# Kernel optimization log

Hardware: AMD Instinct MI355X
Metric: run time of the kernel (lower is better)

The kernel has to match this reference:

```python
import jax, jax.numpy as jnp
import numpy as np

B, T, D, H = 2, 2048, 2048, 16
HD = D // H
EPS = 1e-8
NEG = -1e9


def setup_inputs() -> dict:
    key = jax.random.key(0)
    ks = jax.random.split(key, 6)
    x = jax.random.normal(ks[0], (B, T, D), dtype=jnp.float32)
    # additive causal mask, broadcast over [B, H, T, T]
    causal = jnp.tril(jnp.ones((T, T), dtype=bool))
    attn_mask = jnp.where(causal, 0.0, NEG).astype(jnp.float32)[None, None]
    s = 1.0 / np.sqrt(D)
    w_norm = jnp.ones((D,), dtype=jnp.float32)
    wq = jax.random.normal(ks[1], (D, D), dtype=jnp.float32) * s
    wk = jax.random.normal(ks[2], (D, D), dtype=jnp.float32) * s
    wv = jax.random.normal(ks[3], (D, D), dtype=jnp.float32) * s
    wo = jax.random.normal(ks[4], (D, D), dtype=jnp.float32) * s
    return {"x": x, "attn_mask": attn_mask, "w_norm": w_norm,
            "wq": wq, "wk": wk, "wv": wv, "wo": wo}


def _rmsnorm(x, w):
    # norm = ||x||_2 * D^-0.5 ; out = w * x / (norm + eps)  (eps outside, as in source)
    norm = jnp.sqrt(jnp.sum(x * x, axis=-1, keepdims=True)) * (x.shape[-1] ** -0.5)
    return w * x / (norm + EPS)


def reference(x, attn_mask, w_norm, wq, wk, wv, wo):
    b, t, d = x.shape
    xn = _rmsnorm(x, w_norm)
    # Linear (no bias): y = x @ W^T ; split into heads -> [B, H, T, HD]
    def proj(w):
        return jnp.einsum('btd,ed->bte', xn, w).reshape(b, t, H, HD).transpose(0, 2, 1, 3)
    q, k, v = proj(wq), proj(wk), proj(wv)
    scale = HD ** -0.5
    w_scores = jnp.einsum('bhqd,bhkd->bhqk', q, k) * scale + attn_mask
    p = jax.nn.softmax(w_scores, axis=-1)
    out = jnp.einsum('bhqk,bhkd->bhqd', p, v)
    out = out.transpose(0, 2, 1, 3).reshape(b, t, d)
    return jnp.einsum('btd,ed->bte', out, wo)
```

## Files before the change

kernel.cpp:

```cpp
#include <hip/hip_runtime.h>
#include <stdint.h>

#define TT 2048
#define DD 2048
#define NHH 16
#define HDD 128
#define BTT 4096

typedef __attribute__((ext_vector_type(8))) short bf16x8;
typedef __attribute__((ext_vector_type(4))) float f32x4;

__device__ __forceinline__ unsigned short f2bf(float f) {
    union { float f; uint32_t u; } v; v.f = f;
    uint32_t u = v.u;
    u += 0x7fffu + ((u >> 16) & 1u);
    return (unsigned short)(u >> 16);
}

__device__ __forceinline__ void gld16(const unsigned short* g, unsigned short* l) {
    __builtin_amdgcn_global_load_lds(
        (const __attribute__((address_space(1))) unsigned int*)g,
        (__attribute__((address_space(3))) unsigned int*)l, 16, 0, 0);
}

__global__ __launch_bounds__(256) void convert_w(const float* __restrict__ wq,
                                                 const float* __restrict__ wk,
                                                 const float* __restrict__ wv,
                                                 const float* __restrict__ wo,
                                                 unsigned short* __restrict__ out) {
    size_t gid = (size_t)blockIdx.x * 256 + threadIdx.x;
    size_t base = gid * 8;
    int which = (int)(base >> 22);
    const float* src = which == 0 ? wq : which == 1 ? wk : which == 2 ? wv : wo;
    size_t off = base & 4194303u;
    float4 a = ((const float4*)(src + off))[0];
    float4 b = ((const float4*)(src + off))[1];
    union { unsigned short us[8]; uint4 v; } pk;
    pk.us[0] = f2bf(a.x); pk.us[1] = f2bf(a.y); pk.us[2] = f2bf(a.z); pk.us[3] = f2bf(a.w);
    pk.us[4] = f2bf(b.x); pk.us[5] = f2bf(b.y); pk.us[6] = f2bf(b.z); pk.us[7] = f2bf(b.w);
    *(uint4*)(out + base) = pk.v;
}

__global__ __launch_bounds__(256) void rmsnorm_k(const float* __restrict__ x,
                                                 const float* __restrict__ w,
                                                 unsigned short* __restrict__ xn) {
    const int row = blockIdx.x;
    const int tid = threadIdx.x;
    const float* xr = x + (size_t)row * DD;
    float4 a = ((const float4*)xr)[tid * 2];
    float4 b = ((const float4*)xr)[tid * 2 + 1];
    float ss = a.x*a.x + a.y*a.y + a.z*a.z + a.w*a.w
             + b.x*b.x + b.y*b.y + b.z*b.z + b.w*b.w;
    #pragma unroll
    for (int m = 1; m < 64; m <<= 1) ss += __shfl_xor(ss, m, 64);
    __shared__ float wss[4];
    if ((tid & 63) == 0) wss[tid >> 6] = ss;
    __syncthreads();
    float total = wss[0] + wss[1] + wss[2] + wss[3];
    float norm = sqrtf(total) * 0.022097086912079612f;
    float inv = 1.0f / (norm + 1e-8f);
    float4 wa = ((const float4*)w)[tid * 2];
    float4 wb = ((const float4*)w)[tid * 2 + 1];
    union { unsigned short us[8]; uint4 v; } pk;
    pk.us[0] = f2bf(wa.x * a.x * inv); pk.us[1] = f2bf(wa.y * a.y * inv);
    pk.us[2] = f2bf(wa.z * a.z * inv); pk.us[3] = f2bf(wa.w * a.w * inv);
    pk.us[4] = f2bf(wb.x * b.x * inv); pk.us[5] = f2bf(wb.y * b.y * inv);
    pk.us[6] = f2bf(wb.z * b.z * inv); pk.us[7] = f2bf(wb.w * b.w * inv);
    ((uint4*)(xn + (size_t)row * DD))[tid] = pk.v;
}

__device__ __forceinline__ void gemm_core(const unsigned short* __restrict__ Ag0,
                                          const unsigned short* __restrict__ Bg0,
                                          unsigned short* As, unsigned short* Bs,
                                          int tid, f32x4 acc[4][4]) {
    const int w = tid >> 6, lane = tid & 63;
    const int l15 = lane & 15, lq = lane >> 4;
    const int wr = (w >> 1) * 64, wc = (w & 1) * 64;
    const unsigned short* ag = Ag0 + (size_t)(w * 16 + (lane >> 2)) * DD + (lane & 3) * 8;
    const unsigned short* bg = Bg0 + (size_t)(w * 16 + (lane >> 2)) * DD + (lane & 3) * 8;
    unsigned short* al = As + w * 512;
    unsigned short* bl = Bs + w * 512;
    for (int k0 = 0; k0 < DD; k0 += 32) {
        __syncthreads();
        gld16(ag + k0, al);
        gld16(ag + k0 + (size_t)64 * DD, al + 64 * 32);
        gld16(bg + k0, bl);
        gld16(bg + k0 + (size_t)64 * DD, bl + 64 * 32);
        __syncthreads();
        bf16x8 af[4], bfr[4];
        #pragma unroll
        for (int i = 0; i < 4; i++)
            af[i] = *(const bf16x8*)(As + (wr + i * 16 + l15) * 32 + lq * 8);
        #pragma unroll
        for (int j = 0; j < 4; j++)
            bfr[j] = *(const bf16x8*)(Bs + (wc + j * 16 + l15) * 32 + lq * 8);
        #pragma unroll
        for (int i = 0; i < 4; i++)
            #pragma unroll
            for (int j = 0; j < 4; j++)
                acc[i][j] = __builtin_amdgcn_mfma_f32_16x16x32_bf16(af[i], bfr[j], acc[i][j], 0, 0, 0);
    }
}

__global__ __launch_bounds__(256) void gemm_qkv(const unsigned short* __restrict__ A,
                                                const unsigned short* __restrict__ W3,
                                                unsigned short* __restrict__ O3) {
    __shared__ __align__(16) unsigned short As[128 * 32];
    __shared__ __align__(16) unsigned short Bs[128 * 32];
    const int tid = threadIdx.x;
    const int wave = tid >> 6, lane = tid & 63;
    const int l15 = lane & 15, lq = lane >> 4;
    const int by = blockIdx.y;
    const int which = by >> 4;
    const unsigned short* Bw = W3 + (size_t)which * DD * DD;
    unsigned short* C = O3 + (size_t)which * BTT * DD;
    const int m0 = blockIdx.x * 128, n0 = (by & 15) * 128;
    const int wr = (wave >> 1) * 64, wc = (wave & 1) * 64;
    const f32x4 zf = {0.f, 0.f, 0.f, 0.f};
    f32x4 acc[4][4];
    #pragma unroll
    for (int i = 0; i < 4; i++)
        #pragma unroll
        for (int j = 0; j < 4; j++) acc[i][j] = zf;
    gemm_core(A + (size_t)m0 * DD, Bw + (size_t)n0 * DD, As, Bs, tid, acc);
    #pragma unroll
    for (int i = 0; i < 4; i++) {
        const int row = m0 + wr + i * 16 + lq * 4;
        #pragma unroll
        for (int j = 0; j < 4; j++) {
            const int col = n0 + wc + j * 16 + l15;
            #pragma unroll
            for (int r = 0; r < 4; r++)
                C[(size_t)(row + r) * DD + col] = f2bf(acc[i][j][r]);
        }
    }
}

__global__ __launch_bounds__(256) void gemm_out(const unsigned short* __restrict__ A,
                                                const unsigned short* __restrict__ Bw,
                                                float* __restrict__ C) {
    __shared__ __align__(16) unsigned short As[128 * 32];
    __shared__ __align__(16) unsigned short Bs[128 * 32];
    const int tid = threadIdx.x;
    const int wave = tid >> 6, lane = tid & 63;
    const int l15 = lane & 15, lq = lane >> 4;
    const int m0 = blockIdx.x * 128, n0 = blockIdx.y * 128;
    const int wr = (wave >> 1) * 64, wc = (wave & 1) * 64;
    const f32x4 zf = {0.f, 0.f, 0.f, 0.f};
    f32x4 acc[4][4];
    #pragma unroll
    for (int i = 0; i < 4; i++)
        #pragma unroll
        for (int j = 0; j < 4; j++) acc[i][j] = zf;
    gemm_core(A + (size_t)m0 * DD, Bw + (size_t)n0 * DD, As, Bs, tid, acc);
    #pragma unroll
    for (int i = 0; i < 4; i++) {
        const int row = m0 + wr + i * 16 + lq * 4;
        #pragma unroll
        for (int j = 0; j < 4; j++) {
            const int col = n0 + wc + j * 16 + l15;
            #pragma unroll
            for (int r = 0; r < 4; r++)
                C[(size_t)(row + r) * DD + col] = acc[i][j][r];
        }
    }
}

__global__ __launch_bounds__(256) void attn_fused(const unsigned short* __restrict__ q,
                                                  const unsigned short* __restrict__ k,
                                                  const unsigned short* __restrict__ v,
                                                  unsigned short* __restrict__ o) {
    constexpr int LKK = 136;
    constexpr int LPP = 72;
    __shared__ __align__(16) unsigned short Ks[2][64 * LKK];
    __shared__ __align__(16) unsigned short Vts[128 * 64];
    __shared__ __align__(16) unsigned short Ps[4 * 16 * LPP];
    const int h = blockIdx.y, b = blockIdx.z;
    const int tid = threadIdx.x, wave = tid >> 6, lane = tid & 63;
    const int l15 = lane & 15, lq = lane >> 4;
    const size_t rowbase = (size_t)b * TT;
    const int hcol = h * HDD;
    const float scale = 0.08838834764831845f;
    unsigned short* Pw = Ps + wave * 16 * LPP;
    const f32x4 zf = {0.f, 0.f, 0.f, 0.f};

    uint4 kr0, kr1, kr2, kr3, vr0, vr1, vr2, vr3;
    const int sidx = tid * 8;
    const int srr = sidx >> 7;
    const int sc  = sidx & 127;
    const int swz = ((sc >> 3) & 7) << 3;
    const int srs0 = (srr +  0) ^ swz;
    const int srs1 = (srr + 16) ^ swz;
    const int srs2 = (srr + 32) ^ swz;
    const int srs3 = (srr + 48) ^ swz;

    for (int half = 0; half < 2; half++) {
        const int qj = (half == 0) ? blockIdx.x : 31 - blockIdx.x;
        const int qt0 = qj * 64;
        bf16x8 aq[4];
        {
            const unsigned short* qrp = q + (rowbase + qt0 + wave * 16 + l15) * DD + hcol;
            #pragma unroll
            for (int kk = 0; kk < 4; kk++)
                aq[kk] = *(const bf16x8*)(qrp + kk * 32 + lq * 8);
        }
        f32x4 acc_o[8];
        #pragma unroll
        for (int jh = 0; jh < 8; jh++) acc_o[jh] = zf;
        float m_i[4], l_i[4];
        #pragma unroll
        for (int r = 0; r < 4; r++) { m_i[r] = -1e30f; l_i[r] = 0.f; }
        const int qp0 = qt0 + wave * 16 + lq * 4;
        const int nkt = qj + 1;

        __syncthreads();
        {
            const unsigned short* kg = k + rowbase * DD + hcol;
            const unsigned short* vg = v + rowbase * DD + hcol;
            kr0 = *(const uint4*)(kg + (size_t)(srr +  0) * DD + sc);
            kr1 = *(const uint4*)(kg + (size_t)(srr + 16) * DD + sc);
            kr2 = *(const uint4*)(kg + (size_t)(srr + 32) * DD + sc);
            kr3 = *(const uint4*)(kg + (size_t)(srr + 48) * DD + sc);
            vr0 = *(const uint4*)(vg + (size_t)(srr +  0) * DD + sc);
            vr1 = *(const uint4*)(vg + (size_t)(srr + 16) * DD + sc);
            vr2 = *(const uint4*)(vg + (size_t)(srr + 32) * DD + sc);
            vr3 = *(const uint4*)(vg + (size_t)(srr + 48) * DD + sc);
            unsigned short* ksb = &Ks[0][0];
            *(uint4*)(ksb + (srr +  0) * LKK + sc) = kr0;
            *(uint4*)(ksb + (srr + 16) * LKK + sc) = kr1;
            *(uint4*)(ksb + (srr + 32) * LKK + sc) = kr2;
            *(uint4*)(ksb + (srr + 48) * LKK + sc) = kr3;
            if (nkt > 1) {
                const unsigned short* kg1 = k + (rowbase + 64) * DD + hcol;
                kr0 = *(const uint4*)(kg1 + (size_t)(srr +  0) * DD + sc);
                kr1 = *(const uint4*)(kg1 + (size_t)(srr + 16) * DD + sc);
                kr2 = *(const uint4*)(kg1 + (size_t)(srr + 32) * DD + sc);
                kr3 = *(const uint4*)(kg1 + (size_t)(srr + 48) * DD + sc);
            }
        }

        for (int kt = 0; kt < nkt; kt++) {
            const int cur = kt & 1;
            __syncthreads();
            {
                const unsigned short* d0 = (const unsigned short*)&vr0;
                const unsigned short* d1 = (const unsigned short*)&vr1;
                const unsigned short* d2 = (const unsigned short*)&vr2;
                const unsigned short* d3 = (const unsigned short*)&vr3;
                #pragma unroll
                for (int jj = 0; jj < 8; jj++) {
                    Vts[(sc + jj) * 64 + srs0] = d0[jj];
                    Vts[(sc + jj) * 64 + srs1] = d1[jj];
                    Vts[(sc + jj) * 64 + srs2] = d2[jj];
                    Vts[(sc + jj) * 64 + srs3] = d3[jj];
                }
            }
            if (kt + 1 < nkt) {
                unsigned short* ksb = &Ks[cur ^ 1][0];
                *(uint4*)(ksb + (srr +  0) * LKK + sc) = kr0;
                *(uint4*)(ksb + (srr + 16) * LKK + sc) = kr1;
                *(uint4*)(ksb + (srr + 32) * LKK + sc) = kr2;
                *(uint4*)(ksb + (srr + 48) * LKK + sc) = kr3;
            }
            if (kt + 2 < nkt) {
                const unsigned short* kg = k + (rowbase + (kt + 2) * 64) * DD + hcol;
                kr0 = *(const uint4*)(kg + (size_t)(srr +  0) * DD + sc);
                kr1 = *(const uint4*)(kg + (size_t)(srr + 16) * DD + sc);
                kr2 = *(const uint4*)(kg + (size_t)(srr + 32) * DD + sc);
                kr3 = *(const uint4*)(kg + (size_t)(srr + 48) * DD + sc);
            }
            if (kt + 1 < nkt) {
                const unsigned short* vg = v + (rowbase + (kt + 1) * 64) * DD + hcol;
                vr0 = *(const uint4*)(vg + (size_t)(srr +  0) * DD + sc);
                vr1 = *(const uint4*)(vg + (size_t)(srr + 16) * DD + sc);
                vr2 = *(const uint4*)(vg + (size_t)(srr + 32) * DD + sc);
                vr3 = *(const uint4*)(vg + (size_t)(srr + 48) * DD + sc);
            }
            const unsigned short* ksc = &Ks[cur][0];
            f32x4 accs[4];
            #pragma unroll
            for (int j = 0; j < 4; j++) accs[j] = zf;
            __builtin_amdgcn_s_setprio(1);
            #pragma unroll
            for (int j = 0; j < 4; j++)
                #pragma unroll
                for (int kk = 0; kk < 4; kk++) {
                    bf16x8 bk = *(const bf16x8*)(&ksc[(j * 16 + l15) * LKK + kk * 32 + lq * 8]);
                    accs[j] = __builtin_amdgcn_mfma_f32_16x16x32_bf16(aq[kk], bk, accs[j], 0, 0, 0);
                }
            __builtin_amdgcn_s_setprio(0);
            const int kbase = kt * 64;
            float rowmax[4] = {-1e30f, -1e30f, -1e30f, -1e30f};
            #pragma unroll
            for (int j = 0; j < 4; j++) {
                const int kp = kbase + j * 16 + l15;
                #pragma unroll
                for (int r = 0; r < 4; r++) {
                    float s = accs[j][r] * scale;
                    s = (kp > qp0 + r) ? -1e30f : s;
                    accs[j][r] = s;
                    rowmax[r] = fmaxf(rowmax[r], s);
                }
            }
            #pragma unroll
            for (int r = 0; r < 4; r++) {
                float mx = rowmax[r];
                mx = fmaxf(mx, __shfl_xor(mx, 1, 64));
                mx = fmaxf(mx, __shfl_xor(mx, 2, 64));
                mx = fmaxf(mx, __shfl_xor(mx, 4, 64));
                mx = fmaxf(mx, __shfl_xor(mx, 8, 64));
                float m_new = fmaxf(m_i[r], mx);
                float al = __expf(m_i[r] - m_new);
                m_i[r] = m_new;
                l_i[r] *= al;
                #pragma unroll
                for (int jh = 0; jh < 8; jh++) acc_o[jh][r] *= al;
            }
            float rowsum[4] = {0.f, 0.f, 0.f, 0.f};
            #pragma unroll
            for (int j = 0; j < 4; j++)
                #pragma unroll
                for (int r = 0; r < 4; r++) {
                    float p = __expf(accs[j][r] - m_i[r]);
                    rowsum[r] += p;
                    Pw[(lq * 4 + r) * LPP + j * 16 + l15] = f2bf(p);
                }
            #pragma unroll
            for (int r = 0; r < 4; r++) {
                float s = rowsum[r];
                s += __shfl_xor(s, 1, 64);
                s += __shfl_xor(s, 2, 64);
                s += __shfl_xor(s, 4, 64);
                s += __shfl_xor(s, 8, 64);
                l_i[r] += s;
            }
            __syncthreads();
            bf16x8 ap[2];
            #pragma unroll
            for (int kk = 0; kk < 2; kk++)
                ap[kk] = *(const bf16x8*)(&Pw[l15 * LPP + kk * 32 + lq * 8]);
            __builtin_amdgcn_s_setprio(1);
            #pragma unroll
            for (int jh = 0; jh < 8; jh++) {
                const int hd = jh * 16 + l15;
                const int vswz = ((hd >> 3) & 7) << 3;
                #pragma unroll
                for (int kk = 0; kk < 2; kk++) {
                    bf16x8 bv = *(const bf16x8*)(&Vts[hd * 64 + ((kk * 32 + lq * 8) ^ vswz)]);
                    acc_o[jh] = __builtin_amdgcn_mfma_f32_16x16x32_bf16(ap[kk], bv, acc_o[jh], 0, 0, 0);
                }
            }
            __builtin_amdgcn_s_setprio(0);
        }
        #pragma unroll
        for (int jh = 0; jh < 8; jh++) {
            const int col = hcol + jh * 16 + l15;
            #pragma unroll
            for (int r = 0; r < 4; r++)
                o[(rowbase + qp0 + r) * DD + col] = f2bf(acc_o[jh][r] * (1.0f / l_i[r]));
        }
    }
}

extern "C" void kernel_launch(void* const* d_in, const int* in_sizes, int n_in,
                              void* d_out, int out_size, void* d_ws, size_t ws_size,
                              hipStream_t stream) {
    const float* x      = (const float*)d_in[0];
    const float* w_norm = (const float*)d_in[2];
    const float* wq     = (const float*)d_in[3];
    const float* wk     = (const float*)d_in[4];
    const float* wv     = (const float*)d_in[5];
    const float* wo     = (const float*)d_in[6];

    unsigned short* wbf = (unsigned short*)d_ws;
    unsigned short* xn  = wbf + (size_t)4 * DD * DD;
    unsigned short* qb  = xn + (size_t)BTT * DD;
    unsigned short* kb  = qb + (size_t)BTT * DD;
    unsigned short* vb  = kb + (size_t)BTT * DD;
    unsigned short* ab  = vb + (size_t)BTT * DD;

    convert_w<<<8192, 256, 0, stream>>>(wq, wk, wv, wo, wbf);
    rmsnorm_k<<<BTT, 256, 0, stream>>>(x, w_norm, xn);
    dim3 gqkv(32, 48);
    gemm_qkv<<<gqkv, 256, 0, stream>>>(xn, wbf, qb);
    dim3 gattn(16, NHH, 2);
    attn_fused<<<gattn, 256, 0, stream>>>(qb, kb, vb, ab);
    dim3 gout(32, 16);
    gemm_out<<<gout, 256, 0, stream>>>(ab, wbf + (size_t)3 * DD * DD, (float*)d_out);
}
```

Baseline: 423.8 us.

## Rewrite projection GEMMs with 256x256 tiles, double-buffered swizzled LDS and grid remap

Replaces the 128x128, 4-wave GEMM core with a 256x256, 8-wave core. It uses BK=64, double-buffered 128KB LDS with XOR-swizzled layout, and interleaves global_load_lds prefetch of the next K tile with MFMA quadrants. It also remaps workgroup IDs for L2 locality. The aim is more reuse per loaded byte, less LDS bank conflicts, and overlap of memory with compute in the QKV and output projections. The cost is higher register and LDS pressure and fewer workgroups (384 and 128), which may underfill the 256 CUs for the output GEMM.

Result: slower. 445.8 us (+5.2%).

```diff
diff --git a/kernel.cpp b/kernel.cpp
--- a/kernel.cpp
+++ b/kernel.cpp
@@ -9,6 +9,8 @@
 
 typedef __attribute__((ext_vector_type(8))) short bf16x8;
 typedef __attribute__((ext_vector_type(4))) float f32x4;
+
+#define MF(a, b, c) __builtin_amdgcn_mfma_f32_16x16x32_bf16(a, b, c, 0, 0, 0)
 
 __device__ __forceinline__ unsigned short f2bf(float f) {
     union { float f; uint32_t u; } v; v.f = f;
@@ -69,99 +71,198 @@
     ((uint4*)(xn + (size_t)row * DD))[tid] = pk.v;
 }
 
-__device__ __forceinline__ void gemm_core(const unsigned short* __restrict__ Ag0,
-                                          const unsigned short* __restrict__ Bg0,
-                                          unsigned short* As, unsigned short* Bs,
-                                          int tid, f32x4 acc[4][4]) {
-    const int w = tid >> 6, lane = tid & 63;
-    const int l15 = lane & 15, lq = lane >> 4;
-    const int wr = (w >> 1) * 64, wc = (w & 1) * 64;
-    const unsigned short* ag = Ag0 + (size_t)(w * 16 + (lane >> 2)) * DD + (lane & 3) * 8;
-    const unsigned short* bg = Bg0 + (size_t)(w * 16 + (lane >> 2)) * DD + (lane & 3) * 8;
-    unsigned short* al = As + w * 512;
-    unsigned short* bl = Bs + w * 512;
-    for (int k0 = 0; k0 < DD; k0 += 32) {
-        __syncthreads();
-        gld16(ag + k0, al);
-        gld16(ag + k0 + (size_t)64 * DD, al + 64 * 32);
-        gld16(bg + k0, bl);
-        gld16(bg + k0 + (size_t)64 * DD, bl + 64 * 32);
-        __syncthreads();
-        bf16x8 af[4], bfr[4];
-        #pragma unroll
-        for (int i = 0; i < 4; i++)
-            af[i] = *(const bf16x8*)(As + (wr + i * 16 + l15) * 32 + lq * 8);
-        #pragma unroll
-        for (int j = 0; j < 4; j++)
-            bfr[j] = *(const bf16x8*)(Bs + (wc + j * 16 + l15) * 32 + lq * 8);
-        #pragma unroll
-        for (int i = 0; i < 4; i++)
-            #pragma unroll
-            for (int j = 0; j < 4; j++)
-                acc[i][j] = __builtin_amdgcn_mfma_f32_16x16x32_bf16(af[i], bfr[j], acc[i][j], 0, 0, 0);
-    }
-}
-
-__global__ __launch_bounds__(256) void gemm_qkv(const unsigned short* __restrict__ A,
-                                                const unsigned short* __restrict__ W3,
-                                                unsigned short* __restrict__ O3) {
-    __shared__ __align__(16) unsigned short As[128 * 32];
-    __shared__ __align__(16) unsigned short Bs[128 * 32];
+__device__ __forceinline__ void gemm256_core(const unsigned short* __restrict__ Ag,
+                                             const unsigned short* __restrict__ Bg,
+                                             unsigned short* lds, f32x4 acc[8][4]) {
     const int tid = threadIdx.x;
     const int wave = tid >> 6, lane = tid & 63;
-    const int l15 = lane & 15, lq = lane >> 4;
-    const int by = blockIdx.y;
-    const int which = by >> 4;
+    const int wm = wave >> 2, wn = wave & 3;
+    const int l15 = lane & 15, lq = lane >> 4, r7 = l15 & 7;
+    const int gr = lane >> 3;
+    const size_t goff = (size_t)gr * DD + (size_t)((((lane & 7) ^ gr)) * 8);
+    const int xk0 = (lq ^ r7) * 8;
+    const int xk1 = ((4 + lq) ^ r7) * 8;
+    const int aro = (wm * 128 + l15) * 64;
+    const int bro = 16384 + (wn * 64 + l15) * 64;
+    const int sw16 = wave * 16;
+
+    #pragma unroll
+    for (int c = 0; c < 2; c++) {
+        gld16(Ag + (size_t)(sw16 + c * 8) * DD + goff,       lds + (sw16 + c * 8) * 64);
+        gld16(Ag + (size_t)(128 + sw16 + c * 8) * DD + goff, lds + (128 + sw16 + c * 8) * 64);
+        gld16(Bg + (size_t)(sw16 + c * 8) * DD + goff,       lds + 16384 + (sw16 + c * 8) * 64);
+        gld16(Bg + (size_t)(128 + sw16 + c * 8) * DD + goff, lds + 16384 + (128 + sw16 + c * 8) * 64);
+    }
+    asm volatile("s_waitcnt vmcnt(0)" ::: "memory");
+    __builtin_amdgcn_sched_barrier(0);
+    __builtin_amdgcn_s_barrier();
+
+    for (int kt = 0; kt < DD / 64; kt++) {
+        const int cur = (kt & 1) << 15;
+        const int nxt = cur ^ 32768;
+        const bool hn = (kt + 1 < DD / 64);
+        const int kn = (kt + 1) * 64;
+        const unsigned short* ac = lds + cur + aro;
+        const unsigned short* bc = lds + cur + bro;
+        bf16x8 af[4][2], bA[2][2], bB[2][2];
+
+        #pragma unroll
+        for (int m = 0; m < 4; m++) {
+            af[m][0] = *(const bf16x8*)(ac + m * 1024 + xk0);
+            af[m][1] = *(const bf16x8*)(ac + m * 1024 + xk1);
+        }
+        #pragma unroll
+        for (int n = 0; n < 2; n++) {
+            bA[n][0] = *(const bf16x8*)(bc + n * 1024 + xk0);
+            bA[n][1] = *(const bf16x8*)(bc + n * 1024 + xk1);
+        }
+        if (hn) {
+            gld16(Ag + (size_t)(sw16 + 0) * DD + kn + goff, lds + nxt + (sw16 + 0) * 64);
+            gld16(Ag + (size_t)(sw16 + 8) * DD + kn + goff, lds + nxt + (sw16 + 8) * 64);
+        }
+        __builtin_amdgcn_s_barrier();
+        asm volatile("s_waitcnt lgkmcnt(0)" ::: "memory");
+        __builtin_amdgcn_sched_barrier(0);
+        __builtin_amdgcn_s_setprio(1);
+        #pragma unroll
+        for (int m = 0; m < 4; m++)
+            #pragma unroll
+            for (int n = 0; n < 2; n++) {
+                acc[m][n] = MF(af[m][0], bA[n][0], acc[m][n]);
+                acc[m][n] = MF(af[m][1], bA[n][1], acc[m][n]);
+            }
+        __builtin_amdgcn_s_setprio(0);
+        __builtin_amdgcn_s_barrier();
+
+        #pragma unroll
+        for (int n = 0; n < 2; n++) {
+            bB[n][0] = *(const bf16x8*)(bc + (2 + n) * 1024 + xk0);
+            bB[n][1] = *(const bf16x8*)(bc + (2 + n) * 1024 + xk1);
+        }
+        if (hn) {
+            gld16(Ag + (size_t)(128 + sw16 + 0) * DD + kn + goff, lds + nxt + (128 + sw16 + 0) * 64);
+            gld16(Ag + (size_t)(128 + sw16 + 8) * DD + kn + goff, lds + nxt + (128 + sw16 + 8) * 64);
+        }
+        __builtin_amdgcn_s_barrier();
+        asm volatile("s_waitcnt lgkmcnt(0)" ::: "memory");
+        __builtin_amdgcn_sched_barrier(0);
+        __builtin_amdgcn_s_setprio(1);
+        #pragma unroll
+        for (int m = 0; m < 4; m++)
+            #pragma unroll
+            for (int n = 0; n < 2; n++) {
+                acc[m][2 + n] = MF(af[m][0], bB[n][0], acc[m][2 + n]);
+                acc[m][2 + n] = MF(af[m][1], bB[n][1], acc[m][2 + n]);
+            }
+        __builtin_amdgcn_s_setprio(0);
+        __builtin_amdgcn_s_barrier();
+
+        #pragma unroll
+        for (int m = 0; m < 4; m++) {
+            af[m][0] = *(const bf16x8*)(ac + (4 + m) * 1024 + xk0);
+            af[m][1] = *(const bf16x8*)(ac + (4 + m) * 1024 + xk1);
+        }
+        if (hn) {
+            gld16(Bg + (size_t)(sw16 + 0) * DD + kn + goff, lds + nxt + 16384 + (sw16 + 0) * 64);
+            gld16(Bg + (size_t)(sw16 + 8) * DD + kn + goff, lds + nxt + 16384 + (sw16 + 8) * 64);
+        }
+        __builtin_amdgcn_s_barrier();
+        asm volatile("s_waitcnt lgkmcnt(0)" ::: "memory");
+        __builtin_amdgcn_sched_barrier(0);
+        __builtin_amdgcn_s_setprio(1);
+        #pragma unroll
+        for (int m = 0; m < 4; m++)
+            #pragma unroll
+            for (int n = 0; n < 2; n++) {
+                acc[4 + m][n] = MF(af[m][0], bA[n][0], acc[4 + m][n]);
+                acc[4 + m][n] = MF(af[m][1], bA[n][1], acc[4 + m][n]);
+            }
+        __builtin_amdgcn_s_setprio(0);
+        __builtin_amdgcn_s_barrier();
+
+        if (hn) {
+            gld16(Bg + (size_t)(128 + sw16 + 0) * DD + kn + goff, lds + nxt + 16384 + (128 + sw16 + 0) * 64);
+            gld16(Bg + (size_t)(128 + sw16 + 8) * DD + kn + goff, lds + nxt + 16384 + (128 + sw16 + 8) * 64);
+        }
+        __builtin_amdgcn_s_barrier();
+        __builtin_amdgcn_s_setprio(1);
+        #pragma unroll
+        for (int m = 0; m < 4; m++)
+            #pragma unroll
+            for (int n = 0; n < 2; n++) {
+                acc[4 + m][2 + n] = MF(af[m][0], bB[n][0], acc[4 + m][2 + n]);
+                acc[4 + m][2 + n] = MF(af[m][1], bB[n][1], acc[4 + m][2 + n]);
+            }
+        __builtin_amdgcn_s_setprio(0);
+        asm volatile("s_waitcnt vmcnt(0)" ::: "memory");
+        __builtin_amdgcn_sched_barrier(0);
+        __builtin_amdgcn_s_barrier();
+    }
+}
+
+__global__ __launch_bounds__(512, 2) void gemm_qkv(const unsigned short* __restrict__ A,
+                                                   const unsigned short* __restrict__ W3,
+                                                   unsigned short* __restrict__ O3) {
+    __shared__ __align__(16) unsigned short lds[65536];
+    const int nwg = 384;
+    const int orig = blockIdx.y * 16 + blockIdx.x;
+    const int id = (orig & 7) * (nwg / 8) + (orig >> 3);
+    const int bx = id & 15, byy = id >> 4;
+    const int which = byy >> 3;
     const unsigned short* Bw = W3 + (size_t)which * DD * DD;
     unsigned short* C = O3 + (size_t)which * BTT * DD;
-    const int m0 = blockIdx.x * 128, n0 = (by & 15) * 128;
-    const int wr = (wave >> 1) * 64, wc = (wave & 1) * 64;
+    const int m0 = bx * 256, n0 = (byy & 7) * 256;
     const f32x4 zf = {0.f, 0.f, 0.f, 0.f};
-    f32x4 acc[4][4];
-    #pragma unroll
-    for (int i = 0; i < 4; i++)
-        #pragma unroll
-        for (int j = 0; j < 4; j++) acc[i][j] = zf;
-    gemm_core(A + (size_t)m0 * DD, Bw + (size_t)n0 * DD, As, Bs, tid, acc);
-    #pragma unroll
-    for (int i = 0; i < 4; i++) {
-        const int row = m0 + wr + i * 16 + lq * 4;
-        #pragma unroll
-        for (int j = 0; j < 4; j++) {
-            const int col = n0 + wc + j * 16 + l15;
+    f32x4 acc[8][4];
+    #pragma unroll
+    for (int m = 0; m < 8; m++)
+        #pragma unroll
+        for (int n = 0; n < 4; n++) acc[m][n] = zf;
+    gemm256_core(A + (size_t)m0 * DD, Bw + (size_t)n0 * DD, lds, acc);
+    const int wave = threadIdx.x >> 6, lane = threadIdx.x & 63;
+    const int wm = wave >> 2, wn = wave & 3;
+    const int l15 = lane & 15, lq = lane >> 4;
+    #pragma unroll
+    for (int m = 0; m < 8; m++) {
+        const int row = m0 + wm * 128 + m * 16 + lq * 4;
+        #pragma unroll
+        for (int n = 0; n < 4; n++) {
+            const int col = n0 + wn * 64 + n * 16 + l15;
             #pragma unroll
             for (int r = 0; r < 4; r++)
-                C[(size_t)(row + r) * DD + col] = f2bf(acc[i][j][r]);
+                C[(size_t)(row + r) * DD + col] = f2bf(acc[m][n][r]);
         }
     }
 }
 
-__global__ __launch_bounds__(256) void gemm_out(const unsigned short* __restrict__ A,
-                                                const unsigned short* __restrict__ Bw,
-                                                float* __restrict__ C) {
-    __shared__ __align__(16) unsigned short As[128 * 32];
-    __shared__ __align__(16) unsigned short Bs[128 * 32];
-    const int tid = threadIdx.x;
-    const int wave = tid >> 6, lane = tid & 63;
+__global__ __launch_bounds__(512, 2) void gemm_out(const unsigned short* __restrict__ A,
+                                                   const unsigned short* __restrict__ Bw,
+                                                   float* __restrict__ C) {
+    __shared__ __align__(16) unsigned short lds[65536];
+    const int nwg = 128;
+    const int orig = blockIdx.y * 16 + blockIdx.x;
+    const int id = (orig & 7) * (nwg / 8) + (orig >> 3);
+    const int bx = id & 15, byy = id >> 4;
+    const int m0 = bx * 256, n0 = byy * 256;
+    const f32x4 zf = {0.f, 0.f, 0.f, 0.f};
+    f32x4 acc[8][4];
+    #pragma unroll
+    for (int m = 0; m < 8; m++)
+        #pragma unroll
+        for (int n = 0; n < 4; n++) acc[m][n] = zf;
+    gemm256_core(A + (size_t)m0 * DD, Bw + (size_t)n0 * DD, lds, acc);
+    const int wave = threadIdx.x >> 6, lane = threadIdx.x & 63;
+    const int wm = wave >> 2, wn = wave & 3;
     const int l15 = lane & 15, lq = lane >> 4;
-    const int m0 = blockIdx.x * 128, n0 = blockIdx.y * 128;
-    const int wr = (wave >> 1) * 64, wc = (wave & 1) * 64;
-    const f32x4 zf = {0.f, 0.f, 0.f, 0.f};
-    f32x4 acc[4][4];
-    #pragma unroll
-    for (int i = 0; i < 4; i++)
-        #pragma unroll
-        for (int j = 0; j < 4; j++) acc[i][j] = zf;
-    gemm_core(A + (size_t)m0 * DD, Bw + (size_t)n0 * DD, As, Bs, tid, acc);
-    #pragma unroll
-    for (int i = 0; i < 4; i++) {
-        const int row = m0 + wr + i * 16 + lq * 4;
-        #pragma unroll
-        for (int j = 0; j < 4; j++) {
-            const int col = n0 + wc + j * 16 + l15;
+    #pragma unroll
+    for (int m = 0; m < 8; m++) {
+        const int row = m0 + wm * 128 + m * 16 + lq * 4;
+        #pragma unroll
+        for (int n = 0; n < 4; n++) {
+            const int col = n0 + wn * 64 + n * 16 + l15;
             #pragma unroll
             for (int r = 0; r < 4; r++)
-                C[(size_t)(row + r) * DD + col] = acc[i][j][r];
+                C[(size_t)(row + r) * DD + col] = acc[m][n][r];
         }
     }
 }
@@ -286,7 +387,7 @@
                 #pragma unroll
                 for (int kk = 0; kk < 4; kk++) {
                     bf16x8 bk = *(const bf16x8*)(&ksc[(j * 16 + l15) * LKK + kk * 32 + lq * 8]);
-                    accs[j] = __builtin_amdgcn_mfma_f32_16x16x32_bf16(aq[kk], bk, accs[j], 0, 0, 0);
+                    accs[j] = MF(aq[kk], bk, accs[j]);
                 }
             __builtin_amdgcn_s_setprio(0);
             const int kbase = kt * 64;
@@ -347,7 +448,7 @@
                 #pragma unroll
                 for (int kk = 0; kk < 2; kk++) {
                     bf16x8 bv = *(const bf16x8*)(&Vts[hd * 64 + ((kk * 32 + lq * 8) ^ vswz)]);
-                    acc_o[jh] = __builtin_amdgcn_mfma_f32_16x16x32_bf16(ap[kk], bv, acc_o[jh], 0, 0, 0);
+                    acc_o[jh] = MF(ap[kk], bv, acc_o[jh]);
                 }
             }
             __builtin_amdgcn_s_setprio(0);
@@ -381,10 +482,10 @@
 
     convert_w<<<8192, 256, 0, stream>>>(wq, wk, wv, wo, wbf);
     rmsnorm_k<<<BTT, 256, 0, stream>>>(x, w_norm, xn);
-    dim3 gqkv(32, 48);
-    gemm_qkv<<<gqkv, 256, 0, stream>>>(xn, wbf, qb);
+    dim3 gqkv(16, 24);
+    gemm_qkv<<<gqkv, 512, 0, stream>>>(xn, wbf, qb);
     dim3 gattn(16, NHH, 2);
     attn_fused<<<gattn, 256, 0, stream>>>(qb, kb, vb, ab);
-    dim3 gout(32, 16);
-    gemm_out<<<gout, 256, 0, stream>>>(ab, wbf + (size_t)3 * DD * DD, (float*)d_out);
-}
+    dim3 gout(16, 8);
+    gemm_out<<<gout, 512, 0, stream>>>(ab, wbf + (size_t)3 * DD * DD, (float*)d_out);
+}
```
